# Kernel optimization log

Measured on AMD Instinct MI355X. Metric: run time of the kernel, lower is better.

The kernel has to match this reference:

```python
import jax, jax.numpy as jnp
import numpy as np

N, E, G = 2048, 4096, 128      # nodes, edges, graphs
H, IN, ED = 128, 11, 4         # hidden, input node feat, edge feat
BN_EPS = 1e-5


def setup_inputs() -> dict:
    key = jax.random.key(0)
    ks = iter(jax.random.split(key, 40))
    r = lambda shape, s=0.1: jax.random.normal(next(ks), shape, jnp.float32) * s
    inp = dict(
        x=r((N, IN), 1.0),
        edge_attr=jax.random.uniform(next(ks), (E, ED), jnp.float32),
        edge_index=jax.random.randint(next(ks), (2, E), 0, N).astype(jnp.int32),
        batch=jnp.sort(jax.random.randint(next(ks), (N,), 0, G)).astype(jnp.int32),
        # layer 0 (in=11 -> out=128)
        w1_0=r((ED, H)), b1_0=jnp.zeros(H), w2_0=r((H, IN * H), 0.02), b2_0=jnp.zeros(IN * H),
        root_0=r((IN, H)), bias_0=jnp.zeros(H),
        bn_g0=jnp.ones(H), bn_b0=jnp.zeros(H), bn_m0=r((H,), 0.1),
        bn_v0=jax.random.uniform(next(ks), (H,), jnp.float32, 0.5, 1.5),
        # layers 1..4 stacked (in=out=128)
        w1_s=r((4, ED, H)), b1_s=jnp.zeros((4, H)), w2_s=r((4, H, H * H), 0.02), b2_s=jnp.zeros((4, H * H)),
        root_s=r((4, H, H)), bias_s=jnp.zeros((4, H)),
        bn_gs=jnp.ones((4, H)), bn_bs=jnp.zeros((4, H)), bn_ms=r((4, H), 0.1),
        bn_vs=jax.random.uniform(next(ks), (4, H), jnp.float32, 0.5, 1.5),
        # readout MLP
        lin1_w=r((H, H // 2)), lin1_b=jnp.zeros(H // 2),
        lin2_w=r((H // 2, 1)), lin2_b=jnp.zeros(1),
    )
    return inp


def _nnconv(x, src, dst, edge_attr, w1, b1, w2, b2, root, bias):
    in_c = x.shape[-1]
    h = jax.nn.relu(edge_attr @ w1 + b1)                 # [E, H]
    w_e = (h @ w2 + b2).reshape(-1, in_c, H)             # [E, in, H] per-edge weight
    msg = jnp.einsum('ei,eio->eo', x[src], w_e)          # gather + per-edge matvec
    s = jax.ops.segment_sum(msg, dst, num_segments=N)
    cnt = jax.ops.segment_sum(jnp.ones(dst.shape, x.dtype), dst, num_segments=N)
    aggr = s / jnp.maximum(cnt, 1.0)[:, None]            # scatter-mean
    return aggr + x @ root + bias


def _bn_eval(x, g, b, m, v):
    return (x - m) * jax.lax.rsqrt(v + BN_EPS) * g + b


def reference(x, edge_attr, w1_0, b1_0, w2_0, b2_0, root_0, bias_0,
              bn_g0, bn_b0, bn_m0, bn_v0,
              w1_s, b1_s, w2_s, b2_s, root_s, bias_s,
              bn_gs, bn_bs, bn_ms, bn_vs,
              lin1_w, lin1_b, lin2_w, lin2_b,
              edge_index, batch):
    src, dst = edge_index[0], edge_index[1]
    # layer 0
    h = jax.nn.relu(_bn_eval(
        _nnconv(x, src, dst, edge_attr, w1_0, b1_0, w2_0, b2_0, root_0, bias_0),
        bn_g0, bn_b0, bn_m0, bn_v0))
    # layers 1..4 with residual (dims match)
    for l in range(4):
        h_new = jax.nn.relu(_bn_eval(
            _nnconv(h, src, dst, edge_attr, w1_s[l], b1_s[l], w2_s[l], b2_s[l], root_s[l], bias_s[l]),
            bn_gs[l], bn_bs[l], bn_ms[l], bn_vs[l]))
        h = h + h_new
    # global mean pool over graphs
    gs = jax.ops.segment_sum(h, batch, num_segments=G)
    gc = jax.ops.segment_sum(jnp.ones((N,), h.dtype), batch, num_segments=G)
    g = gs / jnp.maximum(gc, 1.0)[:, None]
    # readout (dropout is identity in eval mode)
    g = jax.nn.relu(g @ lin1_w + lin1_b)
    return g @ lin2_w + lin2_b
```

## Files before the change

kernel.cpp:

```cpp
#include <hip/hip_runtime.h>
#include <cstdint>
#include <cstddef>

#define NN 2048
#define NE 4096
#define NG 128
#define HD 128
#define SKM 16
#define SK0 5
#define NCH 64
#define CHE 64

typedef unsigned short u16;
typedef __attribute__((ext_vector_type(8))) short s16x8;
typedef __attribute__((ext_vector_type(4))) float f32x4;

__device__ inline float b2f(u16 u) {
  return __builtin_bit_cast(float, (unsigned int)u << 16);
}
__device__ inline u16 f2b(float f) {
  __bf16 b = (__bf16)f;
  return __builtin_bit_cast(unsigned short, b);
}

#define GLOAD_LDS16(gptr, lptr)                                                          \
  __builtin_amdgcn_global_load_lds((const __attribute__((address_space(1))) unsigned int*)(gptr), \
                                   (__attribute__((address_space(3))) unsigned int*)(lptr), 16, 0, 0)

__global__ void k_count(const int* __restrict__ dst, int* __restrict__ counts,
                        int* __restrict__ hist) {
  int e = blockIdx.x * 256 + threadIdx.x;
  if (e < NE) {
    int d = dst[e];
    atomicAdd(&counts[d], 1);
    atomicAdd(&hist[(e >> 6) * NN + d], 1);
  }
}

__global__ __launch_bounds__(1024) void k_scan(const int* __restrict__ counts,
                                               int* __restrict__ rowptr) {
  __shared__ int s[NN];
  int t = threadIdx.x;
  s[t] = counts[t];
  s[t + 1024] = counts[t + 1024];
  __syncthreads();
  for (int d = 1; d < NN; d <<= 1) {
    int a0 = s[t], a1 = s[t + 1024];
    int v0 = (t >= d) ? s[t - d] : 0;
    int v1 = (t + 1024 >= d) ? s[t + 1024 - d] : 0;
    __syncthreads();
    s[t] = a0 + v0;
    s[t + 1024] = a1 + v1;
    __syncthreads();
  }
  rowptr[t + 1] = s[t];
  rowptr[t + 1025] = s[t + 1024];
  if (t == 0) rowptr[0] = 0;
}

__global__ void k_chunkscan(const int* __restrict__ hist, const int* __restrict__ rowptr,
                            int* __restrict__ chunkoff) {
  int n = blockIdx.x * 256 + threadIdx.x;
  int running = rowptr[n];
#pragma unroll 8
  for (int c = 0; c < NCH; ++c) {
    chunkoff[c * NN + n] = running;
    running += hist[c * NN + n];
  }
}

__global__ __launch_bounds__(64) void k_fill2(const int* __restrict__ dst,
                                              const int* __restrict__ chunkoff,
                                              int* __restrict__ elist) {
  __shared__ int sd[CHE];
  int c = blockIdx.x, t = threadIdx.x;
  int e = c * CHE + t;
  int dv = dst[e];
  sd[t] = dv;
  __syncthreads();
  int lrank = 0;
  for (int j = 0; j < t; ++j) lrank += (sd[j] == dv) ? 1 : 0;
  elist[chunkoff[c * NN + dv] + lrank] = e;
}

__global__ void k_gbounds(const int* __restrict__ batch, int* __restrict__ gstart) {
  int g = threadIdx.x;
  if (g > NG) return;
  int lo = 0, hi = NN;
  while (lo < hi) { int mid = (lo + hi) >> 1; if (batch[mid] < g) lo = mid + 1; else hi = mid; }
  gstart[g] = lo;
}

__global__ void k_hall(const float* __restrict__ ea,
                       const float* __restrict__ w1_0, const float* __restrict__ b1_0,
                       const float* __restrict__ w1_s, const float* __restrict__ b1_s,
                       u16* __restrict__ hb) {
  int idx = blockIdx.x * 256 + threadIdx.x;
  int c = idx & (HD - 1);
  int e = (idx >> 7) & (NE - 1);
  int l = idx >> 19;
  const float* w1 = (l == 0) ? w1_0 : (w1_s + (size_t)(l - 1) * 4 * HD);
  const float* b1 = (l == 0) ? b1_0 : (b1_s + (size_t)(l - 1) * HD);
  float4 a = *(const float4*)(ea + (size_t)e * 4);
  float v = b1[c] + a.x * w1[c] + a.y * w1[HD + c] + a.z * w1[2 * HD + c] + a.w * w1[3 * HD + c];
  hb[idx] = f2b(fmaxf(v, 0.f));
}

__global__ __launch_bounds__(256) void k_w2t(const float* __restrict__ w2s,
                                             const float* __restrict__ b2s,
                                             u16* __restrict__ w2T) {
  int l = blockIdx.z;
  const float* w2 = w2s + (size_t)l * 16384 * 128;
  const float* b2 = b2s + (size_t)l * 128 * 128;
  u16* out = w2T + (size_t)l * 128 * 16512;
  __shared__ float s[64][65];
  int k0 = blockIdx.x * 64, o0 = blockIdx.y * 64;
  int t = threadIdx.x;
  int r = t >> 4, c = (t & 15) * 4;
#pragma unroll
  for (int it = 0; it < 4; ++it) {
    int kk = k0 + r + it * 16;
    const float* srcp = (kk < 16384) ? (w2 + (size_t)kk * 128 + o0 + c)
                                     : (b2 + (size_t)(kk - 16384) * 128 + o0 + c);
    *(float4*)&s[r + it * 16][c] = *(const float4*)srcp;
  }
  __syncthreads();
#pragma unroll
  for (int it = 0; it < 4; ++it) {
    int o = o0 + r + it * 16;
    u16 pk[4];
#pragma unroll
    for (int j = 0; j < 4; ++j) pk[j] = f2b(s[c + j][r + it * 16]);
    *(unsigned long long*)(out + (size_t)o * 16512 + k0 + c) = *(unsigned long long*)pk;
  }
}

__global__ void k_w2t0(const float* __restrict__ w2_0, const float* __restrict__ b2_0,
                       u16* __restrict__ w2T0) {
  int o = blockIdx.x, t = threadIdx.x;
  for (int kap = t; kap < 2080; kap += 256) {
    int k = kap >> 4, i = kap & 15;
    float v = 0.f;
    if (i < 11) {
      if (k < 128) v = w2_0[(size_t)k * 1408 + i * 128 + o];
      else if (k == 128) v = b2_0[i * 128 + o];
    }
    w2T0[(size_t)o * 2080 + kap] = f2b(v);
  }
}

__global__ void k_padx(const float* __restrict__ x, u16* __restrict__ xb) {
  int idx = blockIdx.x * 256 + threadIdx.x;
  int n = idx >> 4, i = idx & 15;
  xb[idx] = f2b(i < 11 ? x[(size_t)n * 11 + i] : 0.f);
}

__device__ inline s16x8 mulpack(s16x8 x, float h) {
  s16x8 r;
#pragma unroll
  for (int j = 0; j < 8; ++j) {
    float xf = b2f((u16)x[j]);
    r[j] = __builtin_bit_cast(short, (__bf16)(xf * h));
  }
  return r;
}

template <bool L0>
__global__ __launch_bounds__(256, 2) void k_mma(
    const u16* __restrict__ xsb,
    const u16* __restrict__ hb,
    const u16* __restrict__ w2T,
    const int* __restrict__ src,
    u16* __restrict__ msgp) {
  constexpr int KT = L0 ? 2080 : 16512;
  __shared__ u16 hT[130][128];
  __shared__ u16 Bs[2][128][32];

  const int tid = threadIdx.x;
  const int e0 = blockIdx.x * 128;
  const int w = tid >> 6, l = tid & 63, l16 = l & 15, g = l >> 4;
  const int wm0 = w * 32;

  int cb, ncb;
  if constexpr (L0) {
    cb = blockIdx.y * 13; ncb = 13;
  } else {
    int sk = blockIdx.y;
    if (sk < 4) { cb = sk * 33; ncb = 33; }
    else        { cb = 132 + (sk - 4) * 32; ncb = 32; }
  }

  {
    int m = tid >> 4;
    int k0 = (tid & 15) * 8;
#pragma unroll
    for (int it = 0; it < 8; ++it, m += 16) {
      s16x8 v = *(const s16x8*)(hb + (size_t)(e0 + m) * 128 + k0);
#pragma unroll
      for (int j = 0; j < 8; ++j) hT[k0 + j][m] = (u16)v[j];
    }
    if (tid < 128) { hT[128][tid] = 0x3F80; hT[129][tid] = 0; }
  }

  const int eA = e0 + wm0 + l16, eB = eA + 16;
  const int nA = src[eA], nB = src[eB];
  s16x8 xr0[L0 ? 1 : 4], xr1[L0 ? 1 : 4];
  if constexpr (L0) {
    xr0[0] = *(const s16x8*)(xsb + (size_t)nA * 16 + (g & 1) * 8);
    xr1[0] = *(const s16x8*)(xsb + (size_t)nB * 16 + (g & 1) * 8);
  } else {
#pragma unroll
    for (int q = 0; q < 4; ++q) {
      xr0[q] = *(const s16x8*)(xsb + (size_t)nA * 128 + g * 8 + q * 32);
      xr1[q] = *(const s16x8*)(xsb + (size_t)nB * 128 + g * 8 + q * 32);
    }
  }

  auto stageB = [&](int b, int c) {
    const int kap0 = c * 32;
    const int row = w * 32 + (l >> 2);
    const u16* gp = w2T + (size_t)row * KT + kap0 + (l & 3) * 8;
    GLOAD_LDS16(gp, &Bs[b][w * 32][0]);
    const u16* gp2 = gp + (size_t)16 * KT;
    GLOAD_LDS16(gp2, &Bs[b][w * 32 + 16][0]);
  };

  stageB(0, cb);
  __syncthreads();

  f32x4 acc[2][8] = {};
  for (int cc = 0; cc < ncb; ++cc) {
    const int c = cb + cc, buf = cc & 1;
    if (cc + 1 < ncb) stageB(buf ^ 1, c + 1);

    float h0, h1;
    if constexpr (L0) {
      int k = 2 * c + (g >> 1);
      h0 = b2f(hT[k][wm0 + l16]);
      h1 = b2f(hT[k][wm0 + 16 + l16]);
    } else {
      int k = c >> 2;
      h0 = b2f(hT[k][wm0 + l16]);
      h1 = b2f(hT[k][wm0 + 16 + l16]);
    }

    s16x8 xv0, xv1;
    if constexpr (L0) {
      xv0 = xr0[0]; xv1 = xr1[0];
    } else {
      switch (c & 3) {
        case 0: xv0 = xr0[0]; xv1 = xr1[0]; break;
        case 1: xv0 = xr0[1]; xv1 = xr1[1]; break;
        case 2: xv0 = xr0[2]; xv1 = xr1[2]; break;
        default: xv0 = xr0[3]; xv1 = xr1[3]; break;
      }
    }
    s16x8 a0 = mulpack(xv0, h0);
    s16x8 a1 = mulpack(xv1, h1);

#pragma unroll
    for (int nt = 0; nt < 8; ++nt) {
      s16x8 bfr = *(const s16x8*)&Bs[buf][nt * 16 + l16][g * 8];
      acc[0][nt] = __builtin_amdgcn_mfma_f32_16x16x32_bf16(a0, bfr, acc[0][nt], 0, 0, 0);
      acc[1][nt] = __builtin_amdgcn_mfma_f32_16x16x32_bf16(a1, bfr, acc[1][nt], 0, 0, 0);
    }
    __syncthreads();
  }

  u16* mp = msgp + ((size_t)blockIdx.y * NE + e0) * 128;
#pragma unroll
  for (int mt = 0; mt < 2; ++mt)
#pragma unroll
    for (int nt = 0; nt < 8; ++nt)
#pragma unroll
      for (int r = 0; r < 4; ++r) {
        int row = wm0 + mt * 16 + 4 * g + r;
        mp[(size_t)row * 128 + nt * 16 + l16] = f2b(acc[mt][nt][r]);
      }
}

template <int NSK>
__global__ void k_aggr(const u16* __restrict__ msgp, const int* __restrict__ rowptr,
                       const int* __restrict__ elist, float* __restrict__ aggr) {
  int n = blockIdx.x, t = threadIdx.x;
  int beg = rowptr[n], end = rowptr[n + 1];
  float v = 0.f;
  for (int j = beg; j < end; ++j) {
    int e = elist[j];
#pragma unroll
    for (int s = 0; s < NSK; ++s) v += b2f(msgp[((size_t)s * NE + e) * HD + t]);
  }
  aggr[(size_t)n * HD + t] = v / fmaxf((float)(end - beg), 1.f);
}

template <int INR>
__global__ void k_update(const float* __restrict__ aggr, const float* __restrict__ xin,
                         const float* __restrict__ root, const float* __restrict__ bias,
                         const float* __restrict__ bg, const float* __restrict__ bb,
                         const float* __restrict__ bm, const float* __restrict__ bv,
                         const float* __restrict__ h_prev, float* __restrict__ h_out,
                         u16* __restrict__ h_out_bf) {
  int n = blockIdx.x, t = threadIdx.x;
  __shared__ float xr[INR];
  if (t < INR) xr[t] = xin[(size_t)n * INR + t];
  __syncthreads();
  float acc = aggr[(size_t)n * HD + t] + bias[t];
#pragma unroll 8
  for (int k = 0; k < INR; ++k) acc += xr[k] * root[(size_t)k * HD + t];
  float bn = (acc - bm[t]) * rsqrtf(bv[t] + 1e-5f) * bg[t] + bb[t];
  float r = fmaxf(bn, 0.f);
  float val = h_prev ? (h_prev[(size_t)n * HD + t] + r) : r;
  h_out[(size_t)n * HD + t] = val;
  h_out_bf[(size_t)n * HD + t] = f2b(val);
}

__global__ void k_pool(const float* __restrict__ h, const int* __restrict__ gstart,
                       float* __restrict__ pooled) {
  int g = blockIdx.x, t = threadIdx.x;
  int beg = gstart[g], end = gstart[g + 1];
  float v = 0.f;
  for (int n = beg; n < end; ++n) v += h[(size_t)n * HD + t];
  pooled[(size_t)g * HD + t] = v / fmaxf((float)(end - beg), 1.f);
}

__global__ void k_readout(const float* __restrict__ pooled,
                          const float* __restrict__ w1, const float* __restrict__ b1,
                          const float* __restrict__ w2, const float* __restrict__ b2,
                          float* __restrict__ out) {
  int g = blockIdx.x, t = threadIdx.x;
  __shared__ float row[HD];
  row[t] = pooled[(size_t)g * HD + t];
  row[t + 64] = pooled[(size_t)g * HD + t + 64];
  __syncthreads();
  float acc = b1[t];
#pragma unroll 8
  for (int k = 0; k < HD; ++k) acc += row[k] * w1[(size_t)k * 64 + t];
  float v = fmaxf(acc, 0.f) * w2[t];
#pragma unroll
  for (int off = 32; off > 0; off >>= 1) v += __shfl_down(v, off);
  if (t == 0) out[g] = v + b2[0];
}

extern "C" void kernel_launch(void* const* d_in, const int* in_sizes, int n_in,
                              void* d_out, int out_size, void* d_ws, size_t ws_size,
                              hipStream_t stream) {
  const float* x      = (const float*)d_in[0];
  const float* ea     = (const float*)d_in[1];
  const int*   eidx   = (const int*)d_in[2];
  const int*   batch  = (const int*)d_in[3];
  const float* w1_0   = (const float*)d_in[4];
  const float* b1_0   = (const float*)d_in[5];
  const float* w2_0   = (const float*)d_in[6];
  const float* b2_0   = (const float*)d_in[7];
  const float* root_0 = (const float*)d_in[8];
  const float* bias_0 = (const float*)d_in[9];
  const float* bn_g0  = (const float*)d_in[10];
  const float* bn_b0  = (const float*)d_in[11];
  const float* bn_m0  = (const float*)d_in[12];
  const float* bn_v0  = (const float*)d_in[13];
  const float* w1_s   = (const float*)d_in[14];
  const float* b1_s   = (const float*)d_in[15];
  const float* w2_s   = (const float*)d_in[16];
  const float* b2_s   = (const float*)d_in[17];
  const float* root_s = (const float*)d_in[18];
  const float* bias_s = (const float*)d_in[19];
  const float* bn_gs  = (const float*)d_in[20];
  const float* bn_bs  = (const float*)d_in[21];
  const float* bn_ms  = (const float*)d_in[22];
  const float* bn_vs  = (const float*)d_in[23];
  const float* lin1_w = (const float*)d_in[24];
  const float* lin1_b = (const float*)d_in[25];
  const float* lin2_w = (const float*)d_in[26];
  const float* lin2_b = (const float*)d_in[27];
  float* out = (float*)d_out;

  char* wsb = (char*)d_ws;
  size_t off = 0;
  auto alloc = [&](size_t bytes) { void* p = wsb + off; off = (off + bytes + 255) & ~(size_t)255; return p; };
  int*   counts   = (int*)alloc(NN * 4);
  int*   rowptr   = (int*)alloc((NN + 4) * 4);
  int*   elist    = (int*)alloc(NE * 4);
  int*   gstart   = (int*)alloc((NG + 4) * 4);
  int*   hist     = (int*)alloc((size_t)NCH * NN * 4);
  int*   chunkoff = (int*)alloc((size_t)NCH * NN * 4);
  u16*   hbf    = (u16*)alloc((size_t)5 * NE * HD * 2);
  u16*   xbf0   = (u16*)alloc((size_t)NN * 16 * 2);
  u16*   w2T0   = (u16*)alloc((size_t)128 * 2080 * 2);
  u16*   w2T    = (u16*)alloc((size_t)4 * 128 * 16512 * 2);
  float* hnA    = (float*)alloc((size_t)NN * HD * 4);
  float* hnB    = (float*)alloc((size_t)NN * HD * 4);
  u16*   hnAb   = (u16*)alloc((size_t)NN * HD * 2);
  u16*   hnBb   = (u16*)alloc((size_t)NN * HD * 2);
  float* aggr   = (float*)alloc((size_t)NN * HD * 4);
  u16*   msgp   = (u16*)alloc((size_t)SKM * NE * HD * 2);
  float* pooled = (float*)alloc((size_t)NG * HD * 4);

  const int* src = eidx;
  const int* dstp = eidx + NE;

  hipMemsetAsync(counts, 0, NN * 4, stream);
  hipMemsetAsync(hist, 0, (size_t)NCH * NN * 4, stream);
  k_count<<<dim3((NE + 255) / 256), dim3(256), 0, stream>>>(dstp, counts, hist);
  k_scan<<<1, 1024, 0, stream>>>(counts, rowptr);
  k_chunkscan<<<dim3(NN / 256), 256, 0, stream>>>(hist, rowptr, chunkoff);
  k_fill2<<<dim3(NCH), 64, 0, stream>>>(dstp, chunkoff, elist);
  k_gbounds<<<1, 256, 0, stream>>>(batch, gstart);
  k_hall<<<dim3(5 * NE * HD / 256), 256, 0, stream>>>(ea, w1_0, b1_0, w1_s, b1_s, hbf);
  k_padx<<<dim3(NN * 16 / 256), 256, 0, stream>>>(x, xbf0);
  k_w2t0<<<dim3(128), 256, 0, stream>>>(w2_0, b2_0, w2T0);
  k_w2t<<<dim3(16512 / 64, 2, 4), 256, 0, stream>>>(w2_s, b2_s, w2T);

  k_mma<true><<<dim3(NE / 128, SK0), 256, 0, stream>>>(xbf0, hbf, w2T0, src, msgp);
  k_aggr<SK0><<<NN, HD, 0, stream>>>(msgp, rowptr, elist, aggr);
  k_update<11><<<NN, HD, 0, stream>>>(aggr, x, root_0, bias_0, bn_g0, bn_b0, bn_m0, bn_v0,
                                      nullptr, hnA, hnAb);

  float* cur = hnA;  u16* curb = hnAb;
  float* nxt = hnB;  u16* nxtb = hnBb;
  for (int l = 1; l <= 4; ++l) {
    const u16* w2Tl = w2T + (size_t)(l - 1) * 128 * 16512;
    k_mma<false><<<dim3(NE / 128, SKM), 256, 0, stream>>>(
        curb, hbf + (size_t)l * NE * HD, w2Tl, src, msgp);
    k_aggr<SKM><<<NN, HD, 0, stream>>>(msgp, rowptr, elist, aggr);
    k_update<128><<<NN, HD, 0, stream>>>(aggr, cur, root_s + (size_t)(l - 1) * HD * HD,
                                         bias_s + (size_t)(l - 1) * HD,
                                         bn_gs + (size_t)(l - 1) * HD, bn_bs + (size_t)(l - 1) * HD,
                                         bn_ms + (size_t)(l - 1) * HD, bn_vs + (size_t)(l - 1) * HD,
                                         cur, nxt, nxtb);
    float* tf = cur; cur = nxt; nxt = tf;
    u16* tb = curb; curb = nxtb; nxtb = tb;
  }

  k_pool<<<NG, HD, 0, stream>>>(cur, gstart, pooled);
  k_readout<<<NG, 64, 0, stream>>>(pooled, lin1_w, lin1_b, lin2_w, lin2_b, out);
}
```

Baseline: 275.3 us.

## Switch to fp16 MFMA, restructure edge-matmul tiling, fuse small kernels

Result: faster. 255.7 us (-7.1%).

```diff
diff --git a/kernel.cpp b/kernel.cpp
--- a/kernel.cpp
+++ b/kernel.cpp
@@ -12,60 +12,48 @@
 #define CHE 64
 
 typedef unsigned short u16;
-typedef __attribute__((ext_vector_type(8))) short s16x8;
+typedef __attribute__((ext_vector_type(8))) _Float16 f16x8;
 typedef __attribute__((ext_vector_type(4))) float f32x4;
-
-__device__ inline float b2f(u16 u) {
-  return __builtin_bit_cast(float, (unsigned int)u << 16);
-}
-__device__ inline u16 f2b(float f) {
-  __bf16 b = (__bf16)f;
-  return __builtin_bit_cast(unsigned short, b);
-}
 
 #define GLOAD_LDS16(gptr, lptr)                                                          \
   __builtin_amdgcn_global_load_lds((const __attribute__((address_space(1))) unsigned int*)(gptr), \
                                    (__attribute__((address_space(3))) unsigned int*)(lptr), 16, 0, 0)
 
-__global__ void k_count(const int* __restrict__ dst, int* __restrict__ counts,
-                        int* __restrict__ hist) {
+__global__ void k_count(const int* __restrict__ dst, int* __restrict__ hist) {
   int e = blockIdx.x * 256 + threadIdx.x;
-  if (e < NE) {
-    int d = dst[e];
-    atomicAdd(&counts[d], 1);
-    atomicAdd(&hist[(e >> 6) * NN + d], 1);
-  }
-}
-
-__global__ __launch_bounds__(1024) void k_scan(const int* __restrict__ counts,
-                                               int* __restrict__ rowptr) {
+  if (e < NE) atomicAdd(&hist[(e >> 6) * NN + dst[e]], 1);
+}
+
+__global__ __launch_bounds__(1024) void k_scan2(const int* __restrict__ hist,
+                                                int* __restrict__ rowptr,
+                                                int* __restrict__ chunkoff,
+                                                const int* __restrict__ batch,
+                                                int* __restrict__ gstart) {
   __shared__ int s[NN];
   int t = threadIdx.x;
-  s[t] = counts[t];
-  s[t + 1024] = counts[t + 1024];
+  int c0 = 0, c1 = 0;
+  for (int c = 0; c < NCH; ++c) { c0 += hist[c * NN + t]; c1 += hist[c * NN + t + 1024]; }
+  s[t] = c0; s[t + 1024] = c1;
   __syncthreads();
   for (int d = 1; d < NN; d <<= 1) {
     int a0 = s[t], a1 = s[t + 1024];
     int v0 = (t >= d) ? s[t - d] : 0;
     int v1 = (t + 1024 >= d) ? s[t + 1024 - d] : 0;
     __syncthreads();
-    s[t] = a0 + v0;
-    s[t + 1024] = a1 + v1;
+    s[t] = a0 + v0; s[t + 1024] = a1 + v1;
     __syncthreads();
   }
-  rowptr[t + 1] = s[t];
-  rowptr[t + 1025] = s[t + 1024];
+  rowptr[t + 1] = s[t]; rowptr[t + 1025] = s[t + 1024];
   if (t == 0) rowptr[0] = 0;
-}
-
-__global__ void k_chunkscan(const int* __restrict__ hist, const int* __restrict__ rowptr,
-                            int* __restrict__ chunkoff) {
-  int n = blockIdx.x * 256 + threadIdx.x;
-  int running = rowptr[n];
-#pragma unroll 8
+  int run0 = s[t] - c0, run1 = s[t + 1024] - c1;
   for (int c = 0; c < NCH; ++c) {
-    chunkoff[c * NN + n] = running;
-    running += hist[c * NN + n];
+    chunkoff[c * NN + t] = run0;        run0 += hist[c * NN + t];
+    chunkoff[c * NN + t + 1024] = run1; run1 += hist[c * NN + t + 1024];
+  }
+  if (t <= NG) {
+    int lo = 0, hi = NN;
+    while (lo < hi) { int mid = (lo + hi) >> 1; if (batch[mid] < t) lo = mid + 1; else hi = mid; }
+    gstart[t] = lo;
   }
 }
 
@@ -83,36 +71,36 @@
   elist[chunkoff[c * NN + dv] + lrank] = e;
 }
 
-__global__ void k_gbounds(const int* __restrict__ batch, int* __restrict__ gstart) {
-  int g = threadIdx.x;
-  if (g > NG) return;
-  int lo = 0, hi = NN;
-  while (lo < hi) { int mid = (lo + hi) >> 1; if (batch[mid] < g) lo = mid + 1; else hi = mid; }
-  gstart[g] = lo;
-}
-
-__global__ void k_hall(const float* __restrict__ ea,
-                       const float* __restrict__ w1_0, const float* __restrict__ b1_0,
-                       const float* __restrict__ w1_s, const float* __restrict__ b1_s,
-                       u16* __restrict__ hb) {
-  int idx = blockIdx.x * 256 + threadIdx.x;
-  int c = idx & (HD - 1);
-  int e = (idx >> 7) & (NE - 1);
-  int l = idx >> 19;
-  const float* w1 = (l == 0) ? w1_0 : (w1_s + (size_t)(l - 1) * 4 * HD);
-  const float* b1 = (l == 0) ? b1_0 : (b1_s + (size_t)(l - 1) * HD);
-  float4 a = *(const float4*)(ea + (size_t)e * 4);
-  float v = b1[c] + a.x * w1[c] + a.y * w1[HD + c] + a.z * w1[2 * HD + c] + a.w * w1[3 * HD + c];
-  hb[idx] = f2b(fmaxf(v, 0.f));
+__global__ void k_hallpad(const float* __restrict__ ea,
+                          const float* __restrict__ w1_0, const float* __restrict__ b1_0,
+                          const float* __restrict__ w1_s, const float* __restrict__ b1_s,
+                          const float* __restrict__ x,
+                          _Float16* __restrict__ hb, _Float16* __restrict__ x16) {
+  int bid = blockIdx.x;
+  if (bid < 10240) {
+    int idx = bid * 256 + threadIdx.x;
+    int c = idx & (HD - 1);
+    int e = (idx >> 7) & (NE - 1);
+    int l = idx >> 19;
+    const float* w1 = (l == 0) ? w1_0 : (w1_s + (size_t)(l - 1) * 4 * HD);
+    const float* b1 = (l == 0) ? b1_0 : (b1_s + (size_t)(l - 1) * HD);
+    float4 a = *(const float4*)(ea + (size_t)e * 4);
+    float v = b1[c] + a.x * w1[c] + a.y * w1[HD + c] + a.z * w1[2 * HD + c] + a.w * w1[3 * HD + c];
+    hb[idx] = (_Float16)fmaxf(v, 0.f);
+  } else {
+    int idx = (bid - 10240) * 256 + threadIdx.x;
+    int n = idx >> 4, i = idx & 15;
+    x16[idx] = (_Float16)(i < 11 ? x[(size_t)n * 11 + i] : 0.f);
+  }
 }
 
 __global__ __launch_bounds__(256) void k_w2t(const float* __restrict__ w2s,
                                              const float* __restrict__ b2s,
-                                             u16* __restrict__ w2T) {
+                                             _Float16* __restrict__ w2T) {
   int l = blockIdx.z;
   const float* w2 = w2s + (size_t)l * 16384 * 128;
   const float* b2 = b2s + (size_t)l * 128 * 128;
-  u16* out = w2T + (size_t)l * 128 * 16512;
+  _Float16* out = w2T + (size_t)l * 128 * 16512;
   __shared__ float s[64][65];
   int k0 = blockIdx.x * 64, o0 = blockIdx.y * 64;
   int t = threadIdx.x;
@@ -128,15 +116,15 @@
 #pragma unroll
   for (int it = 0; it < 4; ++it) {
     int o = o0 + r + it * 16;
-    u16 pk[4];
-#pragma unroll
-    for (int j = 0; j < 4; ++j) pk[j] = f2b(s[c + j][r + it * 16]);
-    *(unsigned long long*)(out + (size_t)o * 16512 + k0 + c) = *(unsigned long long*)pk;
+    _Float16 pk[4];
+#pragma unroll
+    for (int j = 0; j < 4; ++j) pk[j] = (_Float16)s[c + j][r + it * 16];
+    *(unsigned long long*)(out + (size_t)o * 16512 + k0 + c) = *(const unsigned long long*)pk;
   }
 }
 
 __global__ void k_w2t0(const float* __restrict__ w2_0, const float* __restrict__ b2_0,
-                       u16* __restrict__ w2T0) {
+                       _Float16* __restrict__ w2T0) {
   int o = blockIdx.x, t = threadIdx.x;
   for (int kap = t; kap < 2080; kap += 256) {
     int k = kap >> 4, i = kap & 15;
@@ -145,200 +133,167 @@
       if (k < 128) v = w2_0[(size_t)k * 1408 + i * 128 + o];
       else if (k == 128) v = b2_0[i * 128 + o];
     }
-    w2T0[(size_t)o * 2080 + kap] = f2b(v);
-  }
-}
-
-__global__ void k_padx(const float* __restrict__ x, u16* __restrict__ xb) {
-  int idx = blockIdx.x * 256 + threadIdx.x;
-  int n = idx >> 4, i = idx & 15;
-  xb[idx] = f2b(i < 11 ? x[(size_t)n * 11 + i] : 0.f);
-}
-
-__device__ inline s16x8 mulpack(s16x8 x, float h) {
-  s16x8 r;
-#pragma unroll
-  for (int j = 0; j < 8; ++j) {
-    float xf = b2f((u16)x[j]);
-    r[j] = __builtin_bit_cast(short, (__bf16)(xf * h));
-  }
-  return r;
+    w2T0[(size_t)o * 2080 + kap] = (_Float16)v;
+  }
 }
 
 template <bool L0>
-__global__ __launch_bounds__(256, 2) void k_mma(
-    const u16* __restrict__ xsb,
-    const u16* __restrict__ hb,
-    const u16* __restrict__ w2T,
+__global__ __launch_bounds__(256, 2) void k_mma2(
+    const _Float16* __restrict__ xh,
+    const _Float16* __restrict__ hb,
+    const _Float16* __restrict__ w2T,
     const int* __restrict__ src,
-    u16* __restrict__ msgp) {
+    _Float16* __restrict__ msgp) {
   constexpr int KT = L0 ? 2080 : 16512;
-  __shared__ u16 hT[130][128];
-  __shared__ u16 Bs[2][128][32];
+  constexpr int NWIN = L0 ? 1 : 4;
+  __shared__ _Float16 Bs[2][4096];
+  __shared__ _Float16 hTl[26][128];
 
   const int tid = threadIdx.x;
   const int e0 = blockIdx.x * 128;
   const int w = tid >> 6, l = tid & 63, l16 = l & 15, g = l >> 4;
-  const int wm0 = w * 32;
-
-  int cb, ncb;
+
+  int k0, nk;
   if constexpr (L0) {
-    cb = blockIdx.y * 13; ncb = 13;
+    k0 = blockIdx.y * 13; nk = 13;
   } else {
     int sk = blockIdx.y;
-    if (sk < 4) { cb = sk * 33; ncb = 33; }
-    else        { cb = 132 + (sk - 4) * 32; ncb = 32; }
-  }
+    if (sk == 0) { k0 = 0; nk = 9; } else { k0 = 9 + (sk - 1) * 8; nk = 8; }
+  }
+  const int kb = L0 ? k0 * 2 : k0;
+
+  int nd[8];
+#pragma unroll
+  for (int mt = 0; mt < 8; ++mt) nd[mt] = src[e0 + mt * 16 + l16];
 
   {
-    int m = tid >> 4;
-    int k0 = (tid & 15) * 8;
-#pragma unroll
-    for (int it = 0; it < 8; ++it, m += 16) {
-      s16x8 v = *(const s16x8*)(hb + (size_t)(e0 + m) * 128 + k0);
-#pragma unroll
-      for (int j = 0; j < 8; ++j) hT[k0 + j][m] = (u16)v[j];
-    }
-    if (tid < 128) { hT[128][tid] = 0x3F80; hT[129][tid] = 0; }
-  }
-
-  const int eA = e0 + wm0 + l16, eB = eA + 16;
-  const int nA = src[eA], nB = src[eB];
-  s16x8 xr0[L0 ? 1 : 4], xr1[L0 ? 1 : 4];
-  if constexpr (L0) {
-    xr0[0] = *(const s16x8*)(xsb + (size_t)nA * 16 + (g & 1) * 8);
-    xr1[0] = *(const s16x8*)(xsb + (size_t)nB * 16 + (g & 1) * 8);
-  } else {
-#pragma unroll
-    for (int q = 0; q < 4; ++q) {
-      xr0[q] = *(const s16x8*)(xsb + (size_t)nA * 128 + g * 8 + q * 32);
-      xr1[q] = *(const s16x8*)(xsb + (size_t)nB * 128 + g * 8 + q * 32);
-    }
-  }
-
-  auto stageB = [&](int b, int c) {
-    const int kap0 = c * 32;
-    const int row = w * 32 + (l >> 2);
-    const u16* gp = w2T + (size_t)row * KT + kap0 + (l & 3) * 8;
-    GLOAD_LDS16(gp, &Bs[b][w * 32][0]);
-    const u16* gp2 = gp + (size_t)16 * KT;
-    GLOAD_LDS16(gp2, &Bs[b][w * 32 + 16][0]);
+    const int nrow = L0 ? 26 : nk;
+    for (int idx = tid; idx < nrow * 128; idx += 256) {
+      int kk = idx >> 7, m = idx & 127;
+      int k = kb + kk;
+      _Float16 v;
+      if (k < 128) v = hb[(size_t)(e0 + m) * 128 + k];
+      else v = (k == 128) ? (_Float16)1.0f : (_Float16)0.0f;
+      hTl[kk][m] = v;
+    }
+  }
+
+  auto stageB = [&](int buf, int kap0) {
+#pragma unroll
+    for (int j2 = 0; j2 < 2; ++j2) {
+      int ntg = w * 2 + j2;
+      const _Float16* gp = w2T + (size_t)(ntg * 16 + l16) * KT + kap0 + g * 8;
+      GLOAD_LDS16(gp, &Bs[buf][(w * 128 + j2 * 64) * 8]);
+    }
   };
 
-  stageB(0, cb);
-  __syncthreads();
-
-  f32x4 acc[2][8] = {};
-  for (int cc = 0; cc < ncb; ++cc) {
-    const int c = cb + cc, buf = cc & 1;
-    if (cc + 1 < ncb) stageB(buf ^ 1, c + 1);
-
-    float h0, h1;
-    if constexpr (L0) {
-      int k = 2 * c + (g >> 1);
-      h0 = b2f(hT[k][wm0 + l16]);
-      h1 = b2f(hT[k][wm0 + 16 + l16]);
-    } else {
-      int k = c >> 2;
-      h0 = b2f(hT[k][wm0 + l16]);
-      h1 = b2f(hT[k][wm0 + 16 + l16]);
-    }
-
-    s16x8 xv0, xv1;
-    if constexpr (L0) {
-      xv0 = xr0[0]; xv1 = xr1[0];
-    } else {
-      switch (c & 3) {
-        case 0: xv0 = xr0[0]; xv1 = xr1[0]; break;
-        case 1: xv0 = xr0[1]; xv1 = xr1[1]; break;
-        case 2: xv0 = xr0[2]; xv1 = xr1[2]; break;
-        default: xv0 = xr0[3]; xv1 = xr1[3]; break;
+  stageB(0, L0 ? k0 * 32 : k0 * 128);
+  __syncthreads();
+
+  f32x4 acc[8][2];
+#pragma unroll
+  for (int mt = 0; mt < 8; ++mt)
+#pragma unroll
+    for (int jj = 0; jj < 2; ++jj) acc[mt][jj] = (f32x4){0.f, 0.f, 0.f, 0.f};
+
+  int buf = 0;
+  for (int win = 0; win < NWIN; ++win) {
+    f16x8 xw[8];
+#pragma unroll
+    for (int mt = 0; mt < 8; ++mt) {
+      const _Float16* xp = L0 ? (xh + (size_t)nd[mt] * 16 + (g & 1) * 8)
+                              : (xh + (size_t)nd[mt] * 128 + win * 32 + g * 8);
+      xw[mt] = *(const f16x8*)xp;
+    }
+    for (int j = 0; j < nk; ++j) {
+      const bool last = (j + 1 == nk) && (win + 1 == NWIN);
+      if (j + 1 < nk) {
+        stageB(buf ^ 1, L0 ? (k0 + j + 1) * 32 : (k0 + j + 1) * 128 + win * 32);
+      } else if (win + 1 < NWIN) {
+        stageB(buf ^ 1, k0 * 128 + (win + 1) * 32);
       }
-    }
-    s16x8 a0 = mulpack(xv0, h0);
-    s16x8 a1 = mulpack(xv1, h1);
-
-#pragma unroll
-    for (int nt = 0; nt < 8; ++nt) {
-      s16x8 bfr = *(const s16x8*)&Bs[buf][nt * 16 + l16][g * 8];
-      acc[0][nt] = __builtin_amdgcn_mfma_f32_16x16x32_bf16(a0, bfr, acc[0][nt], 0, 0, 0);
-      acc[1][nt] = __builtin_amdgcn_mfma_f32_16x16x32_bf16(a1, bfr, acc[1][nt], 0, 0, 0);
-    }
-    __syncthreads();
-  }
-
-  u16* mp = msgp + ((size_t)blockIdx.y * NE + e0) * 128;
-#pragma unroll
-  for (int mt = 0; mt < 2; ++mt)
-#pragma unroll
-    for (int nt = 0; nt < 8; ++nt)
+      if (last) { asm volatile("s_waitcnt vmcnt(0)" ::: "memory"); }
+      else      { asm volatile("s_waitcnt vmcnt(2)" ::: "memory"); }
+      __builtin_amdgcn_sched_barrier(0);
+
+      f16x8 bv0 = *(const f16x8*)&Bs[buf][(size_t)(w * 2 + 0) * 512 + l * 8];
+      f16x8 bv1 = *(const f16x8*)&Bs[buf][(size_t)(w * 2 + 1) * 512 + l * 8];
+#pragma unroll
+      for (int mt = 0; mt < 8; ++mt) {
+        _Float16 hh;
+        if constexpr (L0) hh = hTl[2 * j + (g >> 1)][mt * 16 + l16];
+        else              hh = hTl[j][mt * 16 + l16];
+        f16x8 hv = {hh, hh, hh, hh, hh, hh, hh, hh};
+        f16x8 av = xw[mt] * hv;
+        acc[mt][0] = __builtin_amdgcn_mfma_f32_16x16x32_f16(av, bv0, acc[mt][0], 0, 0, 0);
+        acc[mt][1] = __builtin_amdgcn_mfma_f32_16x16x32_f16(av, bv1, acc[mt][1], 0, 0, 0);
+      }
+      buf ^= 1;
+    }
+  }
+
+  _Float16* mp = msgp + ((size_t)blockIdx.y * NE + e0) * 128;
+#pragma unroll
+  for (int mt = 0; mt < 8; ++mt)
+#pragma unroll
+    for (int jj = 0; jj < 2; ++jj)
 #pragma unroll
       for (int r = 0; r < 4; ++r) {
-        int row = wm0 + mt * 16 + 4 * g + r;
-        mp[(size_t)row * 128 + nt * 16 + l16] = f2b(acc[mt][nt][r]);
+        int row = mt * 16 + 4 * g + r;
+        mp[(size_t)row * 128 + w * 32 + jj * 16 + l16] = (_Float16)acc[mt][jj][r];
       }
 }
 
-template <int NSK>
-__global__ void k_aggr(const u16* __restrict__ msgp, const int* __restrict__ rowptr,
-                       const int* __restrict__ elist, float* __restrict__ aggr) {
+template <int INR, int NSK>
+__global__ void k_au(const _Float16* __restrict__ msgp, const int* __restrict__ rowptr,
+                     const int* __restrict__ elist, const float* __restrict__ xin,
+                     const float* __restrict__ root, const float* __restrict__ bias,
+                     const float* __restrict__ bg, const float* __restrict__ bb,
+                     const float* __restrict__ bm, const float* __restrict__ bv,
+                     const float* __restrict__ h_prev, float* __restrict__ h_out,
+                     _Float16* __restrict__ h_out_h) {
   int n = blockIdx.x, t = threadIdx.x;
+  __shared__ float xr[INR];
+  if (t < INR) xr[t] = xin[(size_t)n * INR + t];
   int beg = rowptr[n], end = rowptr[n + 1];
   float v = 0.f;
   for (int j = beg; j < end; ++j) {
     int e = elist[j];
 #pragma unroll
-    for (int s = 0; s < NSK; ++s) v += b2f(msgp[((size_t)s * NE + e) * HD + t]);
-  }
-  aggr[(size_t)n * HD + t] = v / fmaxf((float)(end - beg), 1.f);
-}
-
-template <int INR>
-__global__ void k_update(const float* __restrict__ aggr, const float* __restrict__ xin,
-                         const float* __restrict__ root, const float* __restrict__ bias,
-                         const float* __restrict__ bg, const float* __restrict__ bb,
-                         const float* __restrict__ bm, const float* __restrict__ bv,
-                         const float* __restrict__ h_prev, float* __restrict__ h_out,
-                         u16* __restrict__ h_out_bf) {
-  int n = blockIdx.x, t = threadIdx.x;
-  __shared__ float xr[INR];
-  if (t < INR) xr[t] = xin[(size_t)n * INR + t];
-  __syncthreads();
-  float acc = aggr[(size_t)n * HD + t] + bias[t];
+    for (int s = 0; s < NSK; ++s) v += (float)msgp[((size_t)s * NE + e) * HD + t];
+  }
+  v /= fmaxf((float)(end - beg), 1.f);
+  __syncthreads();
+  float acc = v + bias[t];
 #pragma unroll 8
   for (int k = 0; k < INR; ++k) acc += xr[k] * root[(size_t)k * HD + t];
   float bn = (acc - bm[t]) * rsqrtf(bv[t] + 1e-5f) * bg[t] + bb[t];
   float r = fmaxf(bn, 0.f);
   float val = h_prev ? (h_prev[(size_t)n * HD + t] + r) : r;
   h_out[(size_t)n * HD + t] = val;
-  h_out_bf[(size_t)n * HD + t] = f2b(val);
-}
-
-__global__ void k_pool(const float* __restrict__ h, const int* __restrict__ gstart,
-                       float* __restrict__ pooled) {
+  h_out_h[(size_t)n * HD + t] = (_Float16)val;
+}
+
+__global__ void k_poolread(const float* __restrict__ h, const int* __restrict__ gstart,
+                           const float* __restrict__ w1, const float* __restrict__ b1,
+                           const float* __restrict__ w2, const float* __restrict__ b2,
+                           float* __restrict__ out) {
   int g = blockIdx.x, t = threadIdx.x;
+  __shared__ float row[HD];
   int beg = gstart[g], end = gstart[g + 1];
   float v = 0.f;
   for (int n = beg; n < end; ++n) v += h[(size_t)n * HD + t];
-  pooled[(size_t)g * HD + t] = v / fmaxf((float)(end - beg), 1.f);
-}
-
-__global__ void k_readout(const float* __restrict__ pooled,
-                          const float* __restrict__ w1, const float* __restrict__ b1,
-                          const float* __restrict__ w2, const float* __restrict__ b2,
-                          float* __restrict__ out) {
-  int g = blockIdx.x, t = threadIdx.x;
-  __shared__ float row[HD];
-  row[t] = pooled[(size_t)g * HD + t];
-  row[t + 64] = pooled[(size_t)g * HD + t + 64];
-  __syncthreads();
-  float acc = b1[t];
+  row[t] = v / fmaxf((float)(end - beg), 1.f);
+  __syncthreads();
+  if (t < 64) {
+    float acc = b1[t];
 #pragma unroll 8
-  for (int k = 0; k < HD; ++k) acc += row[k] * w1[(size_t)k * 64 + t];
-  float v = fmaxf(acc, 0.f) * w2[t];
-#pragma unroll
-  for (int off = 32; off > 0; off >>= 1) v += __shfl_down(v, off);
-  if (t == 0) out[g] = v + b2[0];
+    for (int k = 0; k < HD; ++k) acc += row[k] * w1[(size_t)k * 64 + t];
+    float vv = fmaxf(acc, 0.f) * w2[t];
+#pragma unroll
+    for (int off = 32; off > 0; off >>= 1) vv += __shfl_down(vv, off);
+    if (t == 0) out[g] = vv + b2[0];
+  }
 }
 
 extern "C" void kernel_launch(void* const* d_in, const int* in_sizes, int n_in,
@@ -377,60 +332,51 @@
   char* wsb = (char*)d_ws;
   size_t off = 0;
   auto alloc = [&](size_t bytes) { void* p = wsb + off; off = (off + bytes + 255) & ~(size_t)255; return p; };
-  int*   counts   = (int*)alloc(NN * 4);
-  int*   rowptr   = (int*)alloc((NN + 4) * 4);
-  int*   elist    = (int*)alloc(NE * 4);
-  int*   gstart   = (int*)alloc((NG + 4) * 4);
-  int*   hist     = (int*)alloc((size_t)NCH * NN * 4);
-  int*   chunkoff = (int*)alloc((size_t)NCH * NN * 4);
-  u16*   hbf    = (u16*)alloc((size_t)5 * NE * HD * 2);
-  u16*   xbf0   = (u16*)alloc((size_t)NN * 16 * 2);
-  u16*   w2T0   = (u16*)alloc((size_t)128 * 2080 * 2);
-  u16*   w2T    = (u16*)alloc((size_t)4 * 128 * 16512 * 2);
-  float* hnA    = (float*)alloc((size_t)NN * HD * 4);
-  float* hnB    = (float*)alloc((size_t)NN * HD * 4);
-  u16*   hnAb   = (u16*)alloc((size_t)NN * HD * 2);
-  u16*   hnBb   = (u16*)alloc((size_t)NN * HD * 2);
-  float* aggr   = (float*)alloc((size_t)NN * HD * 4);
-  u16*   msgp   = (u16*)alloc((size_t)SKM * NE * HD * 2);
-  float* pooled = (float*)alloc((size_t)NG * HD * 4);
+  int*      rowptr   = (int*)alloc((NN + 4) * 4);
+  int*      elist    = (int*)alloc(NE * 4);
+  int*      gstart   = (int*)alloc((NG + 4) * 4);
+  int*      hist     = (int*)alloc((size_t)NCH * NN * 4);
+  int*      chunkoff = (int*)alloc((size_t)NCH * NN * 4);
+  _Float16* hbf      = (_Float16*)alloc((size_t)5 * NE * HD * 2);
+  _Float16* x16      = (_Float16*)alloc((size_t)NN * 16 * 2);
+  _Float16* w2T0     = (_Float16*)alloc((size_t)128 * 2080 * 2);
+  _Float16* w2T      = (_Float16*)alloc((size_t)4 * 128 * 16512 * 2);
+  float*    hnA      = (float*)alloc((size_t)NN * HD * 4);
+  float*    hnB      = (float*)alloc((size_t)NN * HD * 4);
+  _Float16* hnAh     = (_Float16*)alloc((size_t)NN * HD * 2);
+  _Float16* hnBh     = (_Float16*)alloc((size_t)NN * HD * 2);
+  _Float16* msgp     = (_Float16*)alloc((size_t)SKM * NE * HD * 2);
 
   const int* src = eidx;
   const int* dstp = eidx + NE;
 
-  hipMemsetAsync(counts, 0, NN * 4, stream);
   hipMemsetAsync(hist, 0, (size_t)NCH * NN * 4, stream);
-  k_count<<<dim3((NE + 255) / 256), dim3(256), 0, stream>>>(dstp, counts, hist);
-  k_scan<<<1, 1024, 0, stream>>>(counts, rowptr);
-  k_chunkscan<<<dim3(NN / 256), 256, 0, stream>>>(hist, rowptr, chunkoff);
+  k_count<<<dim3(16), 256, 0, stream>>>(dstp, hist);
+  k_scan2<<<1, 1024, 0, stream>>>(hist, rowptr, chunkoff, batch, gstart);
   k_fill2<<<dim3(NCH), 64, 0, stream>>>(dstp, chunkoff, elist);
-  k_gbounds<<<1, 256, 0, stream>>>(batch, gstart);
-  k_hall<<<dim3(5 * NE * HD / 256), 256, 0, stream>>>(ea, w1_0, b1_0, w1_s, b1_s, hbf);
-  k_padx<<<dim3(NN * 16 / 256), 256, 0, stream>>>(x, xbf0);
+  k_hallpad<<<dim3(10368), 256, 0, stream>>>(ea, w1_0, b1_0, w1_s, b1_s, x, hbf, x16);
   k_w2t0<<<dim3(128), 256, 0, stream>>>(w2_0, b2_0, w2T0);
   k_w2t<<<dim3(16512 / 64, 2, 4), 256, 0, stream>>>(w2_s, b2_s, w2T);
 
-  k_mma<true><<<dim3(NE / 128, SK0), 256, 0, stream>>>(xbf0, hbf, w2T0, src, msgp);
-  k_aggr<SK0><<<NN, HD, 0, stream>>>(msgp, rowptr, elist, aggr);
-  k_update<11><<<NN, HD, 0, stream>>>(aggr, x, root_0, bias_0, bn_g0, bn_b0, bn_m0, bn_v0,
-                                      nullptr, hnA, hnAb);
-
-  float* cur = hnA;  u16* curb = hnAb;
-  float* nxt = hnB;  u16* nxtb = hnBb;
+  k_mma2<true><<<dim3(NE / 128, SK0), 256, 0, stream>>>(x16, hbf, w2T0, src, msgp);
+  k_au<11, SK0><<<NN, HD, 0, stream>>>(msgp, rowptr, elist, x, root_0, bias_0,
+                                       bn_g0, bn_b0, bn_m0, bn_v0, nullptr, hnA, hnAh);
+
+  float* cur = hnA;  _Float16* curh = hnAh;
+  float* nxt = hnB;  _Float16* nxth = hnBh;
   for (int l = 1; l <= 4; ++l) {
-    const u16* w2Tl = w2T + (size_t)(l - 1) * 128 * 16512;
-    k_mma<false><<<dim3(NE / 128, SKM), 256, 0, stream>>>(
-        curb, hbf + (size_t)l * NE * HD, w2Tl, src, msgp);
-    k_aggr<SKM><<<NN, HD, 0, stream>>>(msgp, rowptr, elist, aggr);
-    k_update<128><<<NN, HD, 0, stream>>>(aggr, cur, root_s + (size_t)(l - 1) * HD * HD,
-                                         bias_s + (size_t)(l - 1) * HD,
-                                         bn_gs + (size_t)(l - 1) * HD, bn_bs + (size_t)(l - 1) * HD,
-                                         bn_ms + (size_t)(l - 1) * HD, bn_vs + (size_t)(l - 1) * HD,
-                                         cur, nxt, nxtb);
+    const _Float16* w2Tl = w2T + (size_t)(l - 1) * 128 * 16512;
+    k_mma2<false><<<dim3(NE / 128, SKM), 256, 0, stream>>>(
+        curh, hbf + (size_t)l * NE * HD, w2Tl, src, msgp);
+    k_au<128, SKM><<<NN, HD, 0, stream>>>(msgp, rowptr, elist, cur,
+                                          root_s + (size_t)(l - 1) * HD * HD,
+                                          bias_s + (size_t)(l - 1) * HD,
+                                          bn_gs + (size_t)(l - 1) * HD, bn_bs + (size_t)(l - 1) * HD,
+                                          bn_ms + (size_t)(l - 1) * HD, bn_vs + (size_t)(l - 1) * HD,
+                                          cur, nxt, nxth);
     float* tf = cur; cur = nxt; nxt = tf;
-    u16* tb = curb; curb = nxtb; nxtb = tb;
-  }
-
-  k_pool<<<NG, HD, 0, stream>>>(cur, gstart, pooled);
-  k_readout<<<NG, 64, 0, stream>>>(pooled, lin1_w, lin1_b, lin2_w, lin2_b, out);
-}
+    _Float16* th = curh; curh = nxth; nxth = th;
+  }
+
+  k_poolread<<<NG, HD, 0, stream>>>(cur, gstart, lin1_w, lin1_b, lin2_w, lin2_b, out);
+}
```
